# Kernel tuning notes

Hardware: AMD Instinct MI355X
Metric: run time of the kernel (lower is better)

Reference implementation:

```python
import jax, jax.numpy as jnp
import numpy as np

N = 100000      # nodes
E = 1600000     # edges (avg degree 16)
IN = 128        # in_feats
H = 4           # num_heads
F = 32          # out_feats per head
NEG_SLOPE = 0.2


def setup_inputs() -> dict:
    key = jax.random.key(0)
    k0, k1, k2, k3, k4, k5 = jax.random.split(key, 6)
    feat = jax.random.normal(k0, (N, IN), dtype=jnp.float32)
    # Glorot-ish scaled params
    W = jax.random.normal(k1, (IN, H * F), dtype=jnp.float32) * (1.0 / np.sqrt(IN))
    attn_l = jax.random.normal(k2, (H, F), dtype=jnp.float32) * 0.1
    attn_r = jax.random.normal(k3, (H, F), dtype=jnp.float32) * 0.1
    bias = jnp.zeros((H * F,), dtype=jnp.float32)
    src = jax.random.randint(k4, (E,), 0, N, dtype=jnp.int32)
    dst = jax.random.randint(k5, (E,), 0, N, dtype=jnp.int32)
    return {"feat": feat, "W": W, "attn_l": attn_l, "attn_r": attn_r,
            "bias": bias, "src": src, "dst": dst}


def reference(feat, W, attn_l, attn_r, bias, src, dst):
    # GeMM: projected features, [N, H, F]
    feat_src = (feat @ W).reshape(N, H, F)
    # per-node attention halves, [N, H]
    el = (feat_src * attn_l).sum(-1)
    er = (feat_src * attn_r).sum(-1)
    # per-edge score e_ij = LeakyReLU(el[src] + er[dst]), [E, H]
    e = el[src] + er[dst]
    e = jnp.where(e > 0, e, NEG_SLOPE * e)
    # edge softmax over destination-node segments (numerically stable)
    m = jax.ops.segment_max(e, dst, num_segments=N)          # [N, H]
    ex = jnp.exp(e - m[dst])                                  # [E, H]
    denom = jax.ops.segment_sum(ex, dst, num_segments=N)     # [N, H]
    alpha = ex / jnp.maximum(denom[dst], 1e-9)                # [E, H]
    # weighted SpMM aggregation: sum_j alpha_ij * Wh_j, [N, H, F]
    msg = feat_src[src] * alpha[:, :, None]                   # [E, H, F]
    rst = jax.ops.segment_sum(msg, dst, num_segments=N)      # [N, H, F]
    rst = rst + bias.reshape(1, H, F)
    return rst
```

## Files before the change

### kernel.cpp

```cpp
#include <hip/hip_runtime.h>
#include <hip/hip_fp16.h>

#define IN_F 128
#define HF   128
#define NH   4
#define NF   32

#define NPB       256
#define NPB_SHIFT 8
#define BIN_CHUNK 4096
#define HIST_BLOCKS 256

typedef __attribute__((ext_vector_type(8))) short short8v;
typedef __attribute__((ext_vector_type(4))) float f32x4;

__device__ __forceinline__ unsigned short f32_to_bf16_rtn(float f) {
    unsigned int u = __float_as_uint(f);
    u += 0x7fffu + ((u >> 16) & 1u);
    return (unsigned short)(u >> 16);
}

#define FMA_MIX_LO(acc, pair, w) \
    asm("v_fma_mix_f32 %0, %1, %2, %0 op_sel:[0,0,0] op_sel_hi:[1,0,0]" \
        : "+v"(acc) : "v"(pair), "v"(w))
#define FMA_MIX_HI(acc, pair, w) \
    asm("v_fma_mix_f32 %0, %1, %2, %0 op_sel:[1,0,0] op_sel_hi:[1,0,0]" \
        : "+v"(acc) : "v"(pair), "v"(w))

__global__ void __launch_bounds__(256)
gat_wfrag(const float* __restrict__ W, short8v* __restrict__ wfrag) {
    const int entry = blockIdx.x * 256 + threadIdx.x;
    const int lane = entry & 63;
    const int kb   = (entry >> 6) & 3;
    const int nt   = entry >> 8;
    const int k0   = kb * 32 + (lane >> 4) * 8;
    const int col  = nt * 16 + (lane & 15);
    short8v s;
    #pragma unroll
    for (int j = 0; j < 8; ++j)
        s[j] = (short)f32_to_bf16_rtn(W[(k0 + j) * HF + col]);
    wfrag[entry] = s;
}

__global__ void __launch_bounds__(256)
gat_gemm_hist(const float* __restrict__ feat, const short8v* __restrict__ wfrag,
              const float* __restrict__ attn_l, const float* __restrict__ attn_r,
              unsigned short* __restrict__ feat_src_h,
              float* __restrict__ el, float* __restrict__ er, int N,
              const int* __restrict__ dst, int* __restrict__ bcount,
              int E, int nbuck, int chunk) {
    __shared__ __align__(16) char smem[49152];
    const int t = threadIdx.x;

    if ((int)blockIdx.x < HIST_BLOCKS) {
        int* h = (int*)smem;
        for (int i = t; i < 512; i += 256) h[i] = 0;
        __syncthreads();
        const int e0 = blockIdx.x * chunk;
        const int e1 = min(e0 + chunk, E);
        for (int e = e0 + t; e < e1; e += 256)
            atomicAdd(&h[dst[e] >> NPB_SHIFT], 1);
        __syncthreads();
        for (int b = t; b < nbuck; b += 256)
            if (h[b]) atomicAdd(&bcount[b], h[b]);
        return;
    }

    unsigned short* a_lds = (unsigned short*)smem;
    unsigned short* w_lds = (unsigned short*)(smem + 16384);
    const int lane = t & 63;
    const int wave = t >> 6;
    const int row0b = (blockIdx.x - HIST_BLOCKS) * 64;

    {
        const uint4* wsrc = (const uint4*)wfrag;
        uint4* wdst = (uint4*)w_lds;
        #pragma unroll
        for (int i = 0; i < 8; ++i)
            wdst[i * 256 + t] = wsrc[i * 256 + t];
    }
    #pragma unroll
    for (int i = 0; i < 8; ++i) {
        int idx = i * 256 + t;
        int row = idx >> 5;
        int c4  = idx & 31;
        int srow = min(row0b + row, N - 1);
        float4 f = *(const float4*)(feat + (size_t)srow * IN_F + c4 * 4);
        unsigned int lo = ((unsigned int)f32_to_bf16_rtn(f.y) << 16) | f32_to_bf16_rtn(f.x);
        unsigned int hi = ((unsigned int)f32_to_bf16_rtn(f.w) << 16) | f32_to_bf16_rtn(f.z);
        int kb = c4 >> 3, g = (c4 >> 1) & 3, half = c4 & 1;
        int wv = row >> 4, m = row & 15;
        unsigned int* p = (unsigned int*)a_lds;
        int u = (wv * 4096 + kb * 1024 + g * 256 + m * 16 + half * 8) >> 2;
        p[u]     = lo;
        p[u + 1] = hi;
    }
    __syncthreads();

    const int m = lane & 15;
    const int g = lane >> 4;
    short8v aw[4];
    #pragma unroll
    for (int kb = 0; kb < 4; ++kb)
        aw[kb] = *(const short8v*)&a_lds[wave * 2048 + kb * 512 + g * 128 + m * 8];

    f32x4 acc[8];
    #pragma unroll
    for (int nt = 0; nt < 8; ++nt) acc[nt] = (f32x4){0.f, 0.f, 0.f, 0.f};

    #pragma unroll
    for (int nt = 0; nt < 8; ++nt) {
        #pragma unroll
        for (int kb = 0; kb < 4; ++kb) {
            short8v bw = *(const short8v*)&w_lds[((nt * 4 + kb) * 64 + lane) * 8];
            acc[nt] = __builtin_amdgcn_mfma_f32_16x16x32_bf16(aw[kb], bw, acc[nt], 0, 0, 0);
        }
    }

    float al[8], ar[8];
    #pragma unroll
    for (int nt = 0; nt < 8; ++nt) {
        al[nt] = attn_l[nt * 16 + m];
        ar[nt] = attn_r[nt * 16 + m];
    }

    #pragma unroll
    for (int r = 0; r < 4; ++r) {
        const int row = row0b + wave * 16 + 4 * g + r;
        const bool valid = (row < N);
        if (valid) {
            #pragma unroll
            for (int nt = 0; nt < 8; ++nt)
                feat_src_h[(size_t)row * HF + nt * 16 + m] =
                    __half_as_ushort(__float2half(acc[nt][r]));
        }
        float pl[NH], pr[NH];
        #pragma unroll
        for (int h = 0; h < NH; ++h) {
            pl[h] = acc[2 * h][r] * al[2 * h] + acc[2 * h + 1][r] * al[2 * h + 1];
            pr[h] = acc[2 * h][r] * ar[2 * h] + acc[2 * h + 1][r] * ar[2 * h + 1];
        }
        #pragma unroll
        for (int mask = 1; mask <= 8; mask <<= 1) {
            #pragma unroll
            for (int h = 0; h < NH; ++h) {
                pl[h] += __shfl_xor(pl[h], mask);
                pr[h] += __shfl_xor(pr[h], mask);
            }
        }
        if (valid && m == 0) {
            *(float4*)(el + (size_t)row * NH) = make_float4(pl[0], pl[1], pl[2], pl[3]);
            *(float4*)(er + (size_t)row * NH) = make_float4(pr[0], pr[1], pr[2], pr[3]);
        }
    }
}

__global__ void __launch_bounds__(512)
gat_bucket_scan(const int* __restrict__ bcount, int* __restrict__ bbase,
                int* __restrict__ gcursor, int* __restrict__ offsets,
                int N, int E, int nbuck) {
    __shared__ int buf[512];
    const int t = threadIdx.x;
    int v = (t < nbuck) ? bcount[t] : 0;
    buf[t] = v;
    __syncthreads();
    for (int off = 1; off < 512; off <<= 1) {
        int x = (t >= off) ? buf[t - off] : 0;
        __syncthreads();
        buf[t] += x;
        __syncthreads();
    }
    if (t < nbuck) {
        int base = buf[t] - v;
        bbase[t]   = base;
        gcursor[t] = base;
    }
    if (t == 0) {
        bbase[nbuck] = E;
        offsets[N]   = E;
    }
}

__global__ void __launch_bounds__(256)
gat_bin(const int* __restrict__ src, const int* __restrict__ dst,
        int* __restrict__ gcursor, unsigned int* __restrict__ gpairs, int E) {
    __shared__ unsigned int stage[BIN_CHUNK];
    __shared__ unsigned short buckof[BIN_CHUNK];
    __shared__ int hist[512];
    __shared__ int sc[512];
    __shared__ int basew[512];
    __shared__ int cur[512];
    const int t = threadIdx.x;
    for (int i = t; i < 512; i += 256) hist[i] = 0;
    __syncthreads();
    const int e0  = blockIdx.x * BIN_CHUNK;
    const int cnt = min(BIN_CHUNK, E - e0);
    for (int i = t; i < cnt; i += 256)
        atomicAdd(&hist[dst[e0 + i] >> NPB_SHIFT], 1);
    __syncthreads();
    sc[t]       = hist[t];
    sc[t + 256] = hist[t + 256];
    __syncthreads();
    for (int off = 1; off < 512; off <<= 1) {
        int x0 = (t >= off) ? sc[t - off] : 0;
        int x1 = sc[t + 256 - off];
        __syncthreads();
        sc[t]       += x0;
        sc[t + 256] += x1;
        __syncthreads();
    }
    for (int b = t; b < 512; b += 256) {
        int c  = hist[b];
        int ex = sc[b] - c;
        cur[b] = ex;
        basew[b] = c ? atomicAdd(&gcursor[b], c) : 0;
    }
    __syncthreads();
    for (int i = t; i < cnt; i += 256) {
        unsigned s = (unsigned)src[e0 + i];
        unsigned d = (unsigned)dst[e0 + i];
        int b = (int)(d >> NPB_SHIFT);
        int p = atomicAdd(&cur[b], 1);
        stage[p]  = (s << 8) | (d & (NPB - 1));
        buckof[p] = (unsigned short)b;
    }
    __syncthreads();
    for (int j = t; j < cnt; j += 256) {
        int b  = (int)buckof[j];
        int ex = sc[b] - hist[b];
        gpairs[basew[b] + (j - ex)] = stage[j];
    }
}

__global__ void __launch_bounds__(256)
gat_fine(const unsigned int* __restrict__ gpairs, const int* __restrict__ bbase,
         int* __restrict__ offsets, int* __restrict__ slot, int N) {
    __shared__ int h[NPB];
    __shared__ int buf[NPB];
    __shared__ int cur[NPB];
    const int b     = blockIdx.x;
    const int node0 = b << NPB_SHIFT;
    const int t     = threadIdx.x;
    const int beg = bbase[b];
    const int end = bbase[b + 1];
    h[t] = 0;
    __syncthreads();
    for (int i = beg + t; i < end; i += 256)
        atomicAdd(&h[gpairs[i] & (NPB - 1)], 1);
    __syncthreads();
    int v = h[t];
    buf[t] = v;
    __syncthreads();
    for (int off = 1; off < 256; off <<= 1) {
        int x = (t >= off) ? buf[t - off] : 0;
        __syncthreads();
        buf[t] += x;
        __syncthreads();
    }
    int ex = buf[t] - v;
    if (node0 + t < N) offsets[node0 + t] = beg + ex;
    cur[t] = ex;
    __syncthreads();
    for (int i = beg + t; i < end; i += 256) {
        unsigned pr = gpairs[i];
        int p = atomicAdd(&cur[pr & (NPB - 1)], 1);
        slot[beg + p] = (int)(pr >> 8);
    }
}

__global__ void __launch_bounds__(256)
gat_aggregate(const unsigned short* __restrict__ feat_src_h,
              const float* __restrict__ el, const float* __restrict__ er,
              const int* __restrict__ offsets, const int* __restrict__ slot,
              const float* __restrict__ bias, float* __restrict__ out, int N) {
    __shared__ int   ss[4][64];
    __shared__ float exs[4][256];
    const int lane = threadIdx.x & 63;
    const int wave = threadIdx.x >> 6;
    const int node = blockIdx.x * 4 + wave;
    if (node >= N) return;
    const int start = offsets[node];
    const int end   = offsets[node + 1];
    const int k  = lane & 15;
    const int g  = lane >> 4;
    const int hm = k >> 2;

    const float4 er4 = *(const float4*)(er + (size_t)node * NH);
    float d0 = 0.f, d1 = 0.f, d2 = 0.f, d3 = 0.f;
    float ax0 = 0.f, ax1 = 0.f, ax2 = 0.f, ax3 = 0.f;
    float ax4 = 0.f, ax5 = 0.f, ax6 = 0.f, ax7 = 0.f;
    const unsigned short* fsp = feat_src_h + 8 * k;
    int*   ssw = ss[wave];
    float* exw = exs[wave];

    for (int c = start; c < end; c += 64) {
        int idx = c + lane;
        bool vld = idx < end;
        int s_l = vld ? slot[idx] : 0;
        float4 ev = make_float4(0.f, 0.f, 0.f, 0.f);
        if (vld) ev = *(const float4*)(el + (size_t)s_l * NH);
        float x0 = ev.x + er4.x; x0 = fmaxf(x0, 0.2f * x0);
        float x1 = ev.y + er4.y; x1 = fmaxf(x1, 0.2f * x1);
        float x2 = ev.z + er4.z; x2 = fmaxf(x2, 0.2f * x2);
        float x3 = ev.w + er4.w; x3 = fmaxf(x3, 0.2f * x3);
        float e0 = vld ? __expf(x0) : 0.f;
        float e1 = vld ? __expf(x1) : 0.f;
        float e2 = vld ? __expf(x2) : 0.f;
        float e3 = vld ? __expf(x3) : 0.f;
        d0 += e0; d1 += e1; d2 += e2; d3 += e3;
        ssw[lane] = s_l;
        *(float4*)&exw[lane * 4] = make_float4(e0, e1, e2, e3);
        asm volatile("" ::: "memory");
        const int n = min(64, end - c);
        int j = g;
        for (; j + 4 < n; j += 8) {
            int jB = j + 4;
            int sA = ssw[j];
            int sB = ssw[jB];
            float wA = exw[j * 4 + hm];
            float wB = exw[jB * 4 + hm];
            uint4 uA = *(const uint4*)(fsp + (size_t)sA * HF);
            uint4 uB = *(const uint4*)(fsp + (size_t)sB * HF);
            FMA_MIX_LO(ax0, uA.x, wA); FMA_MIX_LO(ax0, uB.x, wB);
            FMA_MIX_HI(ax1, uA.x, wA); FMA_MIX_HI(ax1, uB.x, wB);
            FMA_MIX_LO(ax2, uA.y, wA); FMA_MIX_LO(ax2, uB.y, wB);
            FMA_MIX_HI(ax3, uA.y, wA); FMA_MIX_HI(ax3, uB.y, wB);
            FMA_MIX_LO(ax4, uA.z, wA); FMA_MIX_LO(ax4, uB.z, wB);
            FMA_MIX_HI(ax5, uA.z, wA); FMA_MIX_HI(ax5, uB.z, wB);
            FMA_MIX_LO(ax6, uA.w, wA); FMA_MIX_LO(ax6, uB.w, wB);
            FMA_MIX_HI(ax7, uA.w, wA); FMA_MIX_HI(ax7, uB.w, wB);
        }
        if (j < n) {
            int sA = ssw[j];
            float wA = exw[j * 4 + hm];
            uint4 uA = *(const uint4*)(fsp + (size_t)sA * HF);
            FMA_MIX_LO(ax0, uA.x, wA);
            FMA_MIX_HI(ax1, uA.x, wA);
            FMA_MIX_LO(ax2, uA.y, wA);
            FMA_MIX_HI(ax3, uA.y, wA);
            FMA_MIX_LO(ax4, uA.z, wA);
            FMA_MIX_HI(ax5, uA.z, wA);
            FMA_MIX_LO(ax6, uA.w, wA);
            FMA_MIX_HI(ax7, uA.w, wA);
        }
        asm volatile("" ::: "memory");
    }

    #pragma unroll
    for (int msk = 16; msk <= 32; msk <<= 1) {
        ax0 += __shfl_xor(ax0, msk); ax1 += __shfl_xor(ax1, msk);
        ax2 += __shfl_xor(ax2, msk); ax3 += __shfl_xor(ax3, msk);
        ax4 += __shfl_xor(ax4, msk); ax5 += __shfl_xor(ax5, msk);
        ax6 += __shfl_xor(ax6, msk); ax7 += __shfl_xor(ax7, msk);
    }

    #pragma unroll
    for (int msk = 1; msk <= 32; msk <<= 1) {
        d0 += __shfl_xor(d0, msk);
        d1 += __shfl_xor(d1, msk);
        d2 += __shfl_xor(d2, msk);
        d3 += __shfl_xor(d3, msk);
    }
    float dh = (hm == 0) ? d0 : (hm == 1) ? d1 : (hm == 2) ? d2 : d3;
    const float inv = 1.0f / fmaxf(dh, 1e-9f);

    if (g == 0) {
        float4 b0 = *(const float4*)(bias + 8 * k);
        float4 b1 = *(const float4*)(bias + 8 * k + 4);
        float4 o0, o1;
        o0.x = ax0 * inv + b0.x; o0.y = ax1 * inv + b0.y;
        o0.z = ax2 * inv + b0.z; o0.w = ax3 * inv + b0.w;
        o1.x = ax4 * inv + b1.x; o1.y = ax5 * inv + b1.y;
        o1.z = ax6 * inv + b1.z; o1.w = ax7 * inv + b1.w;
        *(float4*)(out + (size_t)node * HF + 8 * k)     = o0;
        *(float4*)(out + (size_t)node * HF + 8 * k + 4) = o1;
    }
}

extern "C" void kernel_launch(void* const* d_in, const int* in_sizes, int n_in,
                              void* d_out, int out_size, void* d_ws, size_t ws_size,
                              hipStream_t stream) {
    const float* feat   = (const float*)d_in[0];
    const float* W      = (const float*)d_in[1];
    const float* attn_l = (const float*)d_in[2];
    const float* attn_r = (const float*)d_in[3];
    const float* bias   = (const float*)d_in[4];
    const int*   src    = (const int*)d_in[5];
    const int*   dst    = (const int*)d_in[6];
    float* out = (float*)d_out;

    const int N = in_sizes[0] / IN_F;
    const int E = in_sizes[5];
    const int nbuck = (N + NPB - 1) / NPB;

    char* ws = (char*)d_ws;
    size_t off = 0;
    auto alloc = [&](size_t bytes) -> void* {
        off = (off + 255) & ~(size_t)255;
        void* p = ws + off;
        off += bytes;
        return p;
    };
    unsigned short* feat_src_h = (unsigned short*)alloc((size_t)N * HF * sizeof(unsigned short));
    float* el      = (float*)alloc((size_t)N * NH * sizeof(float));
    float* er      = (float*)alloc((size_t)N * NH * sizeof(float));
    int*   bcount  = (int*)  alloc((size_t)(nbuck + 1) * sizeof(int));
    int*   bbase   = (int*)  alloc((size_t)(nbuck + 1) * sizeof(int));
    int*   gcursor = (int*)  alloc((size_t)nbuck * sizeof(int));
    int*   offsets = (int*)  alloc((size_t)(N + 1) * sizeof(int));
    unsigned int* gpairs = (unsigned int*)alloc((size_t)E * sizeof(unsigned int));
    int*   slot    = (int*)  alloc((size_t)E * sizeof(int));
    short8v* wfrag = (short8v*)alloc((size_t)2048 * sizeof(short8v));

    hipMemsetAsync(bcount, 0, (size_t)(nbuck + 1) * sizeof(int), stream);

    gat_wfrag<<<8, 256, 0, stream>>>(W, wfrag);

    const int gemmBlocks = (N + 63) / 64;
    const int chunk1 = (E + HIST_BLOCKS - 1) / HIST_BLOCKS;
    gat_gemm_hist<<<HIST_BLOCKS + gemmBlocks, 256, 0, stream>>>(
        feat, wfrag, attn_l, attn_r, feat_src_h, el, er, N,
        dst, bcount, E, nbuck, chunk1);

    gat_bucket_scan<<<1, 512, 0, stream>>>(bcount, bbase, gcursor, offsets, N, E, nbuck);
    gat_bin<<<(E + BIN_CHUNK - 1) / BIN_CHUNK, 256, 0, stream>>>(src, dst, gcursor, gpairs, E);
    gat_fine<<<nbuck, 256, 0, stream>>>(gpairs, bbase, offsets, slot, N);

    gat_aggregate<<<(N + 3) / 4, 256, 0, stream>>>(feat_src_h, el, er, offsets, slot, bias, out, N);
}
```

Before: 149.7 us.

## Regroup kernels: fuse W-fragment prep with histogram, and binning with GEMM

Moves the dst histogram into the small W-fragment conversion launch and fuses the edge-binning pass into the GEMM launch as extra blocks. The binning blocks reuse the GEMM kernel's shared-memory buffer. This drops one kernel launch and lets the memory-bound binning overlap the compute-bound GEMM instead of running after it. The histogram now runs before the GEMM rather than alongside it, which moves the serial dependency chain around.

After: 147.1 us. About the same (-1.8%).

```diff
diff --git a/kernel.cpp b/kernel.cpp
--- a/kernel.cpp
+++ b/kernel.cpp
@@ -10,6 +10,7 @@
 #define NPB_SHIFT 8
 #define BIN_CHUNK 4096
 #define HIST_BLOCKS 256
+#define WFRAG_BLOCKS 8
 
 typedef __attribute__((ext_vector_type(8))) short short8v;
 typedef __attribute__((ext_vector_type(4))) float f32x4;
@@ -28,41 +29,120 @@
         : "+v"(acc) : "v"(pair), "v"(w))
 
 __global__ void __launch_bounds__(256)
-gat_wfrag(const float* __restrict__ W, short8v* __restrict__ wfrag) {
-    const int entry = blockIdx.x * 256 + threadIdx.x;
-    const int lane = entry & 63;
-    const int kb   = (entry >> 6) & 3;
-    const int nt   = entry >> 8;
-    const int k0   = kb * 32 + (lane >> 4) * 8;
-    const int col  = nt * 16 + (lane & 15);
-    short8v s;
-    #pragma unroll
-    for (int j = 0; j < 8; ++j)
-        s[j] = (short)f32_to_bf16_rtn(W[(k0 + j) * HF + col]);
-    wfrag[entry] = s;
+gat_wfrag_hist(const float* __restrict__ W, short8v* __restrict__ wfrag,
+               const int* __restrict__ dst, int* __restrict__ bcount,
+               int E, int nbuck, int chunk) {
+    const int t = threadIdx.x;
+    if ((int)blockIdx.x < WFRAG_BLOCKS) {
+        const int entry = blockIdx.x * 256 + t;
+        const int lane = entry & 63;
+        const int kb   = (entry >> 6) & 3;
+        const int nt   = entry >> 8;
+        const int k0   = kb * 32 + (lane >> 4) * 8;
+        const int col  = nt * 16 + (lane & 15);
+        short8v s;
+        #pragma unroll
+        for (int j = 0; j < 8; ++j)
+            s[j] = (short)f32_to_bf16_rtn(W[(k0 + j) * HF + col]);
+        wfrag[entry] = s;
+        return;
+    }
+    __shared__ int h[512];
+    for (int i = t; i < 512; i += 256) h[i] = 0;
+    __syncthreads();
+    const int hb = blockIdx.x - WFRAG_BLOCKS;
+    const int e0 = hb * chunk;
+    const int e1 = min(e0 + chunk, E);
+    for (int e = e0 + t; e < e1; e += 256)
+        atomicAdd(&h[dst[e] >> NPB_SHIFT], 1);
+    __syncthreads();
+    for (int b = t; b < nbuck; b += 256)
+        if (h[b]) atomicAdd(&bcount[b], h[b]);
+}
+
+__global__ void __launch_bounds__(512)
+gat_bucket_scan(const int* __restrict__ bcount, int* __restrict__ bbase,
+                int* __restrict__ gcursor, int* __restrict__ offsets,
+                int N, int E, int nbuck) {
+    __shared__ int buf[512];
+    const int t = threadIdx.x;
+    int v = (t < nbuck) ? bcount[t] : 0;
+    buf[t] = v;
+    __syncthreads();
+    for (int off = 1; off < 512; off <<= 1) {
+        int x = (t >= off) ? buf[t - off] : 0;
+        __syncthreads();
+        buf[t] += x;
+        __syncthreads();
+    }
+    if (t < nbuck) {
+        int base = buf[t] - v;
+        bbase[t]   = base;
+        gcursor[t] = base;
+    }
+    if (t == 0) {
+        bbase[nbuck] = E;
+        offsets[N]   = E;
+    }
 }
 
 __global__ void __launch_bounds__(256)
-gat_gemm_hist(const float* __restrict__ feat, const short8v* __restrict__ wfrag,
-              const float* __restrict__ attn_l, const float* __restrict__ attn_r,
-              unsigned short* __restrict__ feat_src_h,
-              float* __restrict__ el, float* __restrict__ er, int N,
-              const int* __restrict__ dst, int* __restrict__ bcount,
-              int E, int nbuck, int chunk) {
+gat_bin_gemm(const int* __restrict__ src, const int* __restrict__ dst,
+             int* __restrict__ gcursor, unsigned int* __restrict__ gpairs, int E,
+             int nBin,
+             const float* __restrict__ feat, const short8v* __restrict__ wfrag,
+             const float* __restrict__ attn_l, const float* __restrict__ attn_r,
+             unsigned short* __restrict__ feat_src_h,
+             float* __restrict__ el, float* __restrict__ er, int N) {
     __shared__ __align__(16) char smem[49152];
     const int t = threadIdx.x;
 
-    if ((int)blockIdx.x < HIST_BLOCKS) {
-        int* h = (int*)smem;
-        for (int i = t; i < 512; i += 256) h[i] = 0;
-        __syncthreads();
-        const int e0 = blockIdx.x * chunk;
-        const int e1 = min(e0 + chunk, E);
-        for (int e = e0 + t; e < e1; e += 256)
-            atomicAdd(&h[dst[e] >> NPB_SHIFT], 1);
-        __syncthreads();
-        for (int b = t; b < nbuck; b += 256)
-            if (h[b]) atomicAdd(&bcount[b], h[b]);
+    if ((int)blockIdx.x < nBin) {
+        unsigned int*   stage  = (unsigned int*)smem;
+        unsigned short* buckof = (unsigned short*)(smem + 16384);
+        int* hist  = (int*)(smem + 24576);
+        int* sc    = (int*)(smem + 26624);
+        int* basew = (int*)(smem + 28672);
+        int* cur   = (int*)(smem + 30720);
+        for (int i = t; i < 512; i += 256) hist[i] = 0;
+        __syncthreads();
+        const int e0  = blockIdx.x * BIN_CHUNK;
+        const int cnt = min(BIN_CHUNK, E - e0);
+        for (int i = t; i < cnt; i += 256)
+            atomicAdd(&hist[dst[e0 + i] >> NPB_SHIFT], 1);
+        __syncthreads();
+        sc[t]       = hist[t];
+        sc[t + 256] = hist[t + 256];
+        __syncthreads();
+        for (int off = 1; off < 512; off <<= 1) {
+            int x0 = (t >= off) ? sc[t - off] : 0;
+            int x1 = sc[t + 256 - off];
+            __syncthreads();
+            sc[t]       += x0;
+            sc[t + 256] += x1;
+            __syncthreads();
+        }
+        for (int b = t; b < 512; b += 256) {
+            int c  = hist[b];
+            int ex = sc[b] - c;
+            cur[b] = ex;
+            basew[b] = c ? atomicAdd(&gcursor[b], c) : 0;
+        }
+        __syncthreads();
+        for (int i = t; i < cnt; i += 256) {
+            unsigned s = (unsigned)src[e0 + i];
+            unsigned d = (unsigned)dst[e0 + i];
+            int b = (int)(d >> NPB_SHIFT);
+            int p = atomicAdd(&cur[b], 1);
+            stage[p]  = (s << 8) | (d & (NPB - 1));
+            buckof[p] = (unsigned short)b;
+        }
+        __syncthreads();
+        for (int j = t; j < cnt; j += 256) {
+            int b  = (int)buckof[j];
+            int ex = sc[b] - hist[b];
+            gpairs[basew[b] + (j - ex)] = stage[j];
+        }
         return;
     }
 
@@ -70,7 +150,7 @@
     unsigned short* w_lds = (unsigned short*)(smem + 16384);
     const int lane = t & 63;
     const int wave = t >> 6;
-    const int row0b = (blockIdx.x - HIST_BLOCKS) * 64;
+    const int row0b = (blockIdx.x - nBin) * 64;
 
     {
         const uint4* wsrc = (const uint4*)wfrag;
@@ -152,83 +232,6 @@
             *(float4*)(el + (size_t)row * NH) = make_float4(pl[0], pl[1], pl[2], pl[3]);
             *(float4*)(er + (size_t)row * NH) = make_float4(pr[0], pr[1], pr[2], pr[3]);
         }
-    }
-}
-
-__global__ void __launch_bounds__(512)
-gat_bucket_scan(const int* __restrict__ bcount, int* __restrict__ bbase,
-                int* __restrict__ gcursor, int* __restrict__ offsets,
-                int N, int E, int nbuck) {
-    __shared__ int buf[512];
-    const int t = threadIdx.x;
-    int v = (t < nbuck) ? bcount[t] : 0;
-    buf[t] = v;
-    __syncthreads();
-    for (int off = 1; off < 512; off <<= 1) {
-        int x = (t >= off) ? buf[t - off] : 0;
-        __syncthreads();
-        buf[t] += x;
-        __syncthreads();
-    }
-    if (t < nbuck) {
-        int base = buf[t] - v;
-        bbase[t]   = base;
-        gcursor[t] = base;
-    }
-    if (t == 0) {
-        bbase[nbuck] = E;
-        offsets[N]   = E;
-    }
-}
-
-__global__ void __launch_bounds__(256)
-gat_bin(const int* __restrict__ src, const int* __restrict__ dst,
-        int* __restrict__ gcursor, unsigned int* __restrict__ gpairs, int E) {
-    __shared__ unsigned int stage[BIN_CHUNK];
-    __shared__ unsigned short buckof[BIN_CHUNK];
-    __shared__ int hist[512];
-    __shared__ int sc[512];
-    __shared__ int basew[512];
-    __shared__ int cur[512];
-    const int t = threadIdx.x;
-    for (int i = t; i < 512; i += 256) hist[i] = 0;
-    __syncthreads();
-    const int e0  = blockIdx.x * BIN_CHUNK;
-    const int cnt = min(BIN_CHUNK, E - e0);
-    for (int i = t; i < cnt; i += 256)
-        atomicAdd(&hist[dst[e0 + i] >> NPB_SHIFT], 1);
-    __syncthreads();
-    sc[t]       = hist[t];
-    sc[t + 256] = hist[t + 256];
-    __syncthreads();
-    for (int off = 1; off < 512; off <<= 1) {
-        int x0 = (t >= off) ? sc[t - off] : 0;
-        int x1 = sc[t + 256 - off];
-        __syncthreads();
-        sc[t]       += x0;
-        sc[t + 256] += x1;
-        __syncthreads();
-    }
-    for (int b = t; b < 512; b += 256) {
-        int c  = hist[b];
-        int ex = sc[b] - c;
-        cur[b] = ex;
-        basew[b] = c ? atomicAdd(&gcursor[b], c) : 0;
-    }
-    __syncthreads();
-    for (int i = t; i < cnt; i += 256) {
-        unsigned s = (unsigned)src[e0 + i];
-        unsigned d = (unsigned)dst[e0 + i];
-        int b = (int)(d >> NPB_SHIFT);
-        int p = atomicAdd(&cur[b], 1);
-        stage[p]  = (s << 8) | (d & (NPB - 1));
-        buckof[p] = (unsigned short)b;
-    }
-    __syncthreads();
-    for (int j = t; j < cnt; j += 256) {
-        int b  = (int)buckof[j];
-        int ex = sc[b] - hist[b];
-        gpairs[basew[b] + (j - ex)] = stage[j];
     }
 }
 
@@ -414,16 +417,18 @@
 
     hipMemsetAsync(bcount, 0, (size_t)(nbuck + 1) * sizeof(int), stream);
 
-    gat_wfrag<<<8, 256, 0, stream>>>(W, wfrag);
-
+    const int chunk1 = (E + HIST_BLOCKS - 1) / HIST_BLOCKS;
+    gat_wfrag_hist<<<WFRAG_BLOCKS + HIST_BLOCKS, 256, 0, stream>>>(
+        W, wfrag, dst, bcount, E, nbuck, chunk1);
+
+    gat_bucket_scan<<<1, 512, 0, stream>>>(bcount, bbase, gcursor, offsets, N, E, nbuck);
+
+    const int nBin = (E + BIN_CHUNK - 1) / BIN_CHUNK;
     const int gemmBlocks = (N + 63) / 64;
-    const int chunk1 = (E + HIST_BLOCKS - 1) / HIST_BLOCKS;
-    gat_gemm_hist<<<HIST_BLOCKS + gemmBlocks, 256, 0, stream>>>(
-        feat, wfrag, attn_l, attn_r, feat_src_h, el, er, N,
-        dst, bcount, E, nbuck, chunk1);
-
-    gat_bucket_scan<<<1, 512, 0, stream>>>(bcount, bbase, gcursor, offsets, N, E, nbuck);
-    gat_bin<<<(E + BIN_CHUNK - 1) / BIN_CHUNK, 256, 0, stream>>>(src, dst, gcursor, gpairs, E);
+    gat_bin_gemm<<<nBin + gemmBlocks, 256, 0, stream>>>(
+        src, dst, gcursor, gpairs, E, nBin,
+        feat, wfrag, attn_l, attn_r, feat_src_h, el, er, N);
+
     gat_fine<<<nbuck, 256, 0, stream>>>(gpairs, bbase, offsets, slot, N);
 
     gat_aggregate<<<(N + 3) / 4, 256, 0, stream>>>(feat_src_h, el, er, offsets, slot, bias, out, N);
```
